# Kernel tuning notes

Hardware: AMD Instinct MI355X
Metric: run time of the kernel (lower is better)

The kernel has to match this reference:

```python
import jax, jax.numpy as jnp
import numpy as np

N = 50000        # num nodes
E = 800000       # num edges (avg degree 16)
IN_DIM = 64
OUT_DIM = 64
PE_DIM = 24
HEADS = 2
HID = OUT_DIM * HEADS  # 128


def setup_inputs() -> dict:
    key = jax.random.key(0)
    ks = jax.random.split(key, 16)
    std = 0.1  # trunc_normal_(std=0.1) init in the torch module
    return {
        "x": jax.random.normal(ks[0], (N, IN_DIM), jnp.float32),
        "pe_index": jax.random.randint(ks[1], (2, E), 0, N, jnp.int32),
        "pe_val": jax.random.normal(ks[2], (E, PE_DIM), jnp.float32),
        # edge-weight MLP (blocks): input proj, one residual FFN block, final proj
        "W_in": jax.random.normal(ks[3], (PE_DIM, HID), jnp.float32) * std,
        "b_in": jnp.zeros((HID,), jnp.float32),
        "W1": jax.random.normal(ks[4], (HID, HID), jnp.float32) * std,
        "b1": jnp.zeros((HID,), jnp.float32),
        "W2": jax.random.normal(ks[5], (HID, HID), jnp.float32) * std,
        "b2": jnp.zeros((HID,), jnp.float32),
        "W_fin": jax.random.normal(ks[6], (HID, HID), jnp.float32) * std,
        "b_fin": jnp.zeros((HID,), jnp.float32),
        # node feature -> multi-head projection
        "W_x": jax.random.normal(ks[7], (IN_DIM, HID), jnp.float32) * std,
        "b_x": jnp.zeros((HID,), jnp.float32),
        # per-head output bias
        "head_bias": jnp.zeros((1, HEADS, OUT_DIM), jnp.float32),
        # final out projection
        "W_out": jax.random.normal(ks[8], (HID, OUT_DIM), jnp.float32) * std,
        "b_out": jnp.zeros((OUT_DIM,), jnp.float32),
    }


def _edge_mlp(pe, W_in, b_in, W1, b1, W2, b2, W_fin, b_fin):
    # Linear(pe_dim->hid), then residual block [GELU, Linear, GELU, Linear, +res], then Linear(hid->hid)
    g = lambda t: jax.nn.gelu(t, approximate=False)  # torch nn.GELU default = exact erf
    x0 = pe @ W_in + b_in                     # [E, HID]
    h = g(x0) @ W1 + b1
    h = g(h) @ W2 + b2
    x0 = h + x0                               # ResidualLayer: x + x_res
    return x0 @ W_fin + b_fin                 # [E, HID]


def reference(x, pe_index, pe_val, W_in, b_in, W1, b1, W2, b2, W_fin, b_fin,
              W_x, b_x, head_bias, W_out, b_out):
    tgt = pe_index[0]  # messages aggregate to edge_index[0]
    src = pe_index[1]
    score = _edge_mlp(pe_val, W_in, b_in, W1, b1, W2, b2, W_fin, b_fin)
    score = score.reshape(-1, HEADS, OUT_DIM)                 # [E, H, D]
    xh = (x @ W_x + b_x).reshape(-1, HEADS, OUT_DIM)          # [N, H, D]
    msg = xh[src] * score                                     # gather-multiply
    wV = jax.ops.segment_sum(msg, tgt, num_segments=N)        # scatter-add [N, H, D]
    deg = jax.ops.segment_sum(jnp.ones((msg.shape[0],), jnp.float32), tgt, num_segments=N)
    wV = wV / jnp.maximum(deg, 1.0)[:, None, None]            # average=True -> mean aggregation
    h = (wV + head_bias).reshape(-1, HEADS * OUT_DIM)
    return h @ W_out + b_out                                  # out_proj: [N, OUT_DIM]
```

## Files before the change

kernel.cpp:

```cpp
#include <hip/hip_runtime.h>
#include <hip/hip_bf16.h>
#include <math.h>

#define NN 50000
#define EE 800000
#define HID 128
#define PED 24
#define IND 64
#define OUTD 64
#define EBLK 64
#define AKS 136

typedef short bf16x8 __attribute__((ext_vector_type(8)));
typedef float f32x4 __attribute__((ext_vector_type(4)));

__device__ __forceinline__ float gelu_fast(float x) {
    float z = fabsf(x) * 0.70710678118654752440f;
    float t = __builtin_amdgcn_rcpf(1.0f + 0.3275911f * z);
    float poly = t * (0.254829592f +
                 t * (-0.284496736f +
                 t * (1.421413741f +
                 t * (-1.453152027f +
                 t * 1.061405429f))));
    float e = __expf(-z * z);
    float erfa = 1.0f - poly * e;
    float s = copysignf(erfa, x);
    return 0.5f * x * (1.0f + s);
}
__device__ __forceinline__ unsigned short f2bf(float f) {
    unsigned int u = __float_as_uint(f);
    u = (u + 0x7fffu + ((u >> 16) & 1u)) >> 16;
    return (unsigned short)u;
}
__device__ __forceinline__ unsigned int pkbf2(float a, float b) {
    __hip_bfloat162 h = __float22bfloat162_rn(make_float2(a, b));
    return *reinterpret_cast<unsigned int*>(&h);
}
__device__ __forceinline__ float bflo(unsigned int u) {
    return __uint_as_float(u << 16);
}
__device__ __forceinline__ float bfhi(unsigned int u) {
    return __uint_as_float(u & 0xffff0000u);
}

__global__ __launch_bounds__(256) void xh_kernel(
    const float* __restrict__ x, const float* __restrict__ W_x,
    const float* __restrict__ b_x, unsigned short* __restrict__ xhb) {
    int gid = blockIdx.x * 256 + threadIdx.x;
    int n = gid >> 5;
    int q = gid & 31;
    if (n >= NN) return;
    const float* xr = x + (size_t)n * IND;
    float4 acc = *(const float4*)&b_x[q * 4];
#pragma unroll 8
    for (int k = 0; k < IND; k++) {
        float xk = xr[k];
        float4 w = *(const float4*)&W_x[k * HID + q * 4];
        acc.x += xk * w.x; acc.y += xk * w.y;
        acc.z += xk * w.z; acc.w += xk * w.w;
    }
    uint2 p;
    p.x = pkbf2(acc.x, acc.y);
    p.y = pkbf2(acc.z, acc.w);
    ((uint2*)&xhb[(size_t)n * HID])[q] = p;
}

__global__ __launch_bounds__(256) void prep_kernel(
    const float* __restrict__ W_in, const float* __restrict__ W1,
    const float* __restrict__ W2, const float* __restrict__ Wf,
    unsigned short* __restrict__ WT_in, unsigned short* __restrict__ WT1,
    unsigned short* __restrict__ WT2, unsigned short* __restrict__ WTf) {
    int idx = blockIdx.x * 256 + threadIdx.x;
    if (idx < 4096) {
        int j = idx >> 5, k = idx & 31;
        WT_in[idx] = f2bf(k < PED ? W_in[k * HID + j] : 0.f);
    } else if (idx < 4096 + 16384) {
        int i = idx - 4096; int j = i >> 7, k = i & 127;
        WT1[i] = f2bf(W1[k * HID + j]);
    } else if (idx < 4096 + 32768) {
        int i = idx - 4096 - 16384; int j = i >> 7, k = i & 127;
        WT2[i] = f2bf(W2[k * HID + j]);
    } else if (idx < 4096 + 49152) {
        int i = idx - 4096 - 32768; int j = i >> 7, k = i & 127;
        WTf[i] = f2bf(Wf[k * HID + j]);
    }
}

__global__ __launch_bounds__(256) void hist_kernel(const int* __restrict__ pe_idx,
                                                   int* __restrict__ cnt) {
    int e = blockIdx.x * 256 + threadIdx.x;
    if (e < EE) atomicAdd(&cnt[pe_idx[e]], 1);
}

__global__ __launch_bounds__(1024) void scan_kernel(const int* __restrict__ cnt,
                                                    int* __restrict__ woff) {
    __shared__ int s_w[16];
    int tid = threadIdx.x;
    const int chunk = (NN + 1023) / 1024;
    int base = tid * chunk;
    int end = base + chunk; if (end > NN) end = NN;
    int s = 0;
    for (int i = base; i < end; i++) s += cnt[i];
    int v = s;
    int lane = tid & 63, wid = tid >> 6;
#pragma unroll
    for (int d = 1; d < 64; d <<= 1) {
        int u = __shfl_up(v, d, 64);
        if (lane >= d) v += u;
    }
    if (lane == 63) s_w[wid] = v;
    __syncthreads();
    if (tid < 16) {
        int wv = s_w[tid];
#pragma unroll
        for (int d = 1; d < 16; d <<= 1) {
            int u = __shfl_up(wv, d, 64);
            if (tid >= d) wv += u;
        }
        s_w[tid] = wv;
    }
    __syncthreads();
    int exc = v - s + (wid ? s_w[wid - 1] : 0);
    int run = exc;
    for (int i = base; i < end; i++) { woff[i] = run; run += cnt[i]; }
}

__global__ __launch_bounds__(256) void scatter_kernel(const int* __restrict__ pe_idx,
                                                      int* __restrict__ woff,
                                                      int* __restrict__ perm) {
    int e = blockIdx.x * 256 + threadIdx.x;
    if (e < EE) {
        int t = pe_idx[e];
        int p = atomicAdd(&woff[t], 1);
        perm[p] = e;
    }
}

__global__ __launch_bounds__(256, 3) void edge_kernel(
    const float* __restrict__ pe_val, const int* __restrict__ pe_idx,
    const int* __restrict__ perm, const unsigned short* __restrict__ xhb,
    const unsigned short* __restrict__ WT_in, const unsigned short* __restrict__ WT1,
    const unsigned short* __restrict__ WT2, const unsigned short* __restrict__ WTf,
    const float* __restrict__ b_in, const float* __restrict__ b1,
    const float* __restrict__ b2, const float* __restrict__ bfin,
    float* __restrict__ wV) {
    __shared__ unsigned short s_act[EBLK][AKS];
    __shared__ __align__(16) unsigned short s_W[HID][AKS];
    __shared__ int s_eid[EBLK], s_tgt[EBLK], s_src[EBLK];
    float* s_msg = (float*)&s_W[0][0];

    const int tid = threadIdx.x;
    const int lane = tid & 63;
    const int w = tid >> 6;
    const int l15 = lane & 15;
    const int quad = lane >> 4;
    const long b0 = (long)blockIdx.x * EBLK;

    if (tid < EBLK) {
        int eid = perm[b0 + tid];
        s_eid[tid] = eid;
        s_tgt[tid] = pe_idx[eid];
        s_src[tid] = pe_idx[EE + eid];
    }
#pragma unroll
    for (int i = 0; i < 8; i++) {
        int idx = tid + i * 256; int r = idx >> 4, seg = idx & 15;
        *(uint4*)&s_W[r][seg * 8] = *(const uint4*)&WT1[r * HID + seg * 8];
    }
    __syncthreads();
#pragma unroll
    for (int i = 0; i < 8; i++) {
        int idx = tid + i * 256; int e = idx >> 5, k = idx & 31;
        float v = (k < PED) ? pe_val[(size_t)s_eid[e] * PED + k] : 0.f;
        s_act[e][k] = f2bf(v);
    }
    __syncthreads();

    f32x4 C[2][4];
    f32x4 x0s[2][4];
    const f32x4 z4 = {0.f, 0.f, 0.f, 0.f};

    {
        bf16x8 a0 = *(const bf16x8*)&WT_in[((2 * w + 0) * 16 + l15) * 32 + quad * 8];
        bf16x8 a1 = *(const bf16x8*)&WT_in[((2 * w + 1) * 16 + l15) * 32 + quad * 8];
#pragma unroll
        for (int u = 0; u < 4; u++) {
            bf16x8 bfr = *(const bf16x8*)&s_act[u * 16 + l15][quad * 8];
            C[0][u] = __builtin_amdgcn_mfma_f32_16x16x32_bf16(a0, bfr, z4, 0, 0, 0);
            C[1][u] = __builtin_amdgcn_mfma_f32_16x16x32_bf16(a1, bfr, z4, 0, 0, 0);
        }
    }
    __syncthreads();
#pragma unroll
    for (int t = 0; t < 2; t++) {
        int ch0 = (2 * w + t) * 16 + quad * 4;
        float4 bb = *(const float4*)&b_in[ch0];
#pragma unroll
        for (int u = 0; u < 4; u++) {
            int e = u * 16 + l15;
            f32x4 c = C[t][u];
            c[0] += bb.x; c[1] += bb.y; c[2] += bb.z; c[3] += bb.w;
            x0s[t][u] = c;
            uint2 p;
            p.x = pkbf2(gelu_fast(c[0]), gelu_fast(c[1]));
            p.y = pkbf2(gelu_fast(c[2]), gelu_fast(c[3]));
            *(uint2*)&s_act[e][ch0] = p;
        }
    }
    __syncthreads();

#define GEMM128()                                                              \
    {                                                                          \
        _Pragma("unroll") for (int t = 0; t < 2; t++)                          \
            _Pragma("unroll") for (int u = 0; u < 4; u++) C[t][u] = z4;        \
        _Pragma("unroll") for (int ks = 0; ks < 4; ks++) {                     \
            bf16x8 a0 = *(const bf16x8*)&s_W[(2 * w + 0) * 16 + l15]           \
                                            [ks * 32 + quad * 8];              \
            bf16x8 a1 = *(const bf16x8*)&s_W[(2 * w + 1) * 16 + l15]           \
                                            [ks * 32 + quad * 8];              \
            _Pragma("unroll") for (int u = 0; u < 4; u++) {                    \
                bf16x8 bfr = *(const bf16x8*)&s_act[u * 16 + l15]              \
                                                   [ks * 32 + quad * 8];       \
                C[0][u] = __builtin_amdgcn_mfma_f32_16x16x32_bf16(a0, bfr,     \
                                                                  C[0][u], 0, 0, 0); \
                C[1][u] = __builtin_amdgcn_mfma_f32_16x16x32_bf16(a1, bfr,     \
                                                                  C[1][u], 0, 0, 0); \
            }                                                                  \
        }                                                                      \
    }

#define STAGE_W(WT)                                                            \
    _Pragma("unroll") for (int i = 0; i < 8; i++) {                            \
        int idx = tid + i * 256; int r = idx >> 4, seg = idx & 15;             \
        *(uint4*)&s_W[r][seg * 8] = *(const uint4*)&(WT)[r * HID + seg * 8];   \
    }

    GEMM128();
    __syncthreads();
#pragma unroll
    for (int t = 0; t < 2; t++) {
        int ch0 = (2 * w + t) * 16 + quad * 4;
        float4 bb = *(const float4*)&b1[ch0];
#pragma unroll
        for (int u = 0; u < 4; u++) {
            int e = u * 16 + l15;
            f32x4 c = C[t][u];
            uint2 p;
            p.x = pkbf2(gelu_fast(c[0] + bb.x), gelu_fast(c[1] + bb.y));
            p.y = pkbf2(gelu_fast(c[2] + bb.z), gelu_fast(c[3] + bb.w));
            *(uint2*)&s_act[e][ch0] = p;
        }
    }
    STAGE_W(WT2);
    __syncthreads();

    GEMM128();
    __syncthreads();
#pragma unroll
    for (int t = 0; t < 2; t++) {
        int ch0 = (2 * w + t) * 16 + quad * 4;
        float4 bb = *(const float4*)&b2[ch0];
#pragma unroll
        for (int u = 0; u < 4; u++) {
            int e = u * 16 + l15;
            f32x4 c = C[t][u];
            f32x4 x0 = x0s[t][u];
            uint2 p;
            p.x = pkbf2(c[0] + bb.x + x0[0], c[1] + bb.y + x0[1]);
            p.y = pkbf2(c[2] + bb.z + x0[2], c[3] + bb.w + x0[3]);
            *(uint2*)&s_act[e][ch0] = p;
        }
    }
    STAGE_W(WTf);
    __syncthreads();

    GEMM128();
    __syncthreads();
#pragma unroll
    for (int t = 0; t < 2; t++) {
        int ch0 = (2 * w + t) * 16 + quad * 4;
        float4 bb = *(const float4*)&bfin[ch0];
#pragma unroll
        for (int u = 0; u < 4; u++) {
            int e = u * 16 + l15;
            f32x4 c = C[t][u];
            uint2 p;
            p.x = pkbf2(c[0] + bb.x, c[1] + bb.y);
            p.y = pkbf2(c[2] + bb.z, c[3] + bb.w);
            *(uint2*)&s_act[e][ch0] = p;
        }
    }
    __syncthreads();

#pragma unroll
    for (int i = 0; i < 8; i++) {
        int idx = tid + i * 256;
        int e = idx >> 5, c4 = idx & 31;
        int src = s_src[e];
        uint2 xv = ((const uint2*)&xhb[(size_t)src * HID])[c4];
        uint2 sv = *(const uint2*)&s_act[e][c4 * 4];
        float4 m;
        m.x = bflo(xv.x) * bflo(sv.x);
        m.y = bfhi(xv.x) * bfhi(sv.x);
        m.z = bflo(xv.y) * bflo(sv.y);
        m.w = bfhi(xv.y) * bfhi(sv.y);
        *(float4*)&s_msg[e * HID + c4 * 4] = m;
    }
    __syncthreads();

    {
        const int h = tid >> 7;
        const int c = tid & 127;
        const int e0h = h * 32;
        float acc = 0.f;
        int prev = s_tgt[e0h];
        bool firstseg = true;
        for (int e = e0h; e < e0h + 32; e++) {
            int t = s_tgt[e];
            if (t != prev) {
                if (firstseg) atomicAdd(&wV[(size_t)prev * HID + c], acc);
                else          wV[(size_t)prev * HID + c] = acc;
                firstseg = false;
                acc = 0.f;
                prev = t;
            }
            acc += s_msg[e * HID + c];
        }
        atomicAdd(&wV[(size_t)prev * HID + c], acc);
    }
#undef GEMM128
#undef STAGE_W
}

__global__ __launch_bounds__(256) void out_kernel(
    const float* __restrict__ wV, const int* __restrict__ cnt,
    const float* __restrict__ head_bias, const float* __restrict__ W_out,
    const float* __restrict__ b_out, float* __restrict__ out) {
    int gid = blockIdx.x * 256 + threadIdx.x;
    int n = gid >> 4;
    int q = gid & 15;
    if (n >= NN) return;
    float inv = 1.0f / fmaxf((float)cnt[n], 1.0f);
    const float* wr = wV + (size_t)n * HID;
    float4 acc = *(const float4*)&b_out[q * 4];
#pragma unroll 4
    for (int k = 0; k < HID; k++) {
        float hv = wr[k] * inv + head_bias[k];
        float4 wv4 = *(const float4*)&W_out[k * OUTD + q * 4];
        acc.x += hv * wv4.x; acc.y += hv * wv4.y;
        acc.z += hv * wv4.z; acc.w += hv * wv4.w;
    }
    *(float4*)&out[(size_t)n * OUTD + q * 4] = acc;
}

extern "C" void kernel_launch(void* const* d_in, const int* in_sizes, int n_in,
                              void* d_out, int out_size, void* d_ws, size_t ws_size,
                              hipStream_t stream) {
    const float* x      = (const float*)d_in[0];
    const int*   pe_idx = (const int*)d_in[1];
    const float* pe_val = (const float*)d_in[2];
    const float* W_in   = (const float*)d_in[3];
    const float* b_in   = (const float*)d_in[4];
    const float* W1     = (const float*)d_in[5];
    const float* b1     = (const float*)d_in[6];
    const float* W2     = (const float*)d_in[7];
    const float* b2     = (const float*)d_in[8];
    const float* Wf     = (const float*)d_in[9];
    const float* bfin   = (const float*)d_in[10];
    const float* W_x    = (const float*)d_in[11];
    const float* b_x    = (const float*)d_in[12];
    const float* hb     = (const float*)d_in[13];
    const float* W_out  = (const float*)d_in[14];
    const float* b_out  = (const float*)d_in[15];
    float* out = (float*)d_out;

    float* wV   = (float*)d_ws;
    int*   cnt  = (int*)(wV + (size_t)NN * HID);
    int*   woff = cnt + NN;
    int*   perm = woff + NN;
    unsigned short* WT_in = (unsigned short*)(perm + EE);
    unsigned short* WT1   = WT_in + 128 * 32;
    unsigned short* WT2   = WT1 + 128 * 128;
    unsigned short* WTf   = WT2 + 128 * 128;
    unsigned short* xhb   = WTf + 128 * 128;

    hipMemsetAsync(wV, 0, ((size_t)NN * HID + NN) * sizeof(float), stream);

    hist_kernel<<<(EE + 255) / 256, 256, 0, stream>>>(pe_idx, cnt);
    scan_kernel<<<1, 1024, 0, stream>>>(cnt, woff);
    scatter_kernel<<<(EE + 255) / 256, 256, 0, stream>>>(pe_idx, woff, perm);
    prep_kernel<<<208, 256, 0, stream>>>(W_in, W1, W2, Wf, WT_in, WT1, WT2, WTf);
    xh_kernel<<<(NN * 32 + 255) / 256, 256, 0, stream>>>(x, W_x, b_x, xhb);

    edge_kernel<<<EE / EBLK, 256, 0, stream>>>(pe_val, pe_idx, perm, xhb,
                                               WT_in, WT1, WT2, WTf,
                                               b_in, b1, b2, bfin, wV);

    out_kernel<<<(NN * 16 + 255) / 256, 256, 0, stream>>>(wV, cnt, hb, W_out,
                                                          b_out, out);
}
```

Baseline: 691.9 us.

## Fuse prep kernels, double edge tile, use tanh GELU, fold biases into MFMA

```diff
diff --git a/kernel.cpp b/kernel.cpp
--- a/kernel.cpp
+++ b/kernel.cpp
@@ -8,24 +8,17 @@
 #define PED 24
 #define IND 64
 #define OUTD 64
-#define EBLK 64
+#define EBLK 128
 #define AKS 136
 
 typedef short bf16x8 __attribute__((ext_vector_type(8)));
 typedef float f32x4 __attribute__((ext_vector_type(4)));
 
 __device__ __forceinline__ float gelu_fast(float x) {
-    float z = fabsf(x) * 0.70710678118654752440f;
-    float t = __builtin_amdgcn_rcpf(1.0f + 0.3275911f * z);
-    float poly = t * (0.254829592f +
-                 t * (-0.284496736f +
-                 t * (1.421413741f +
-                 t * (-1.453152027f +
-                 t * 1.061405429f))));
-    float e = __expf(-z * z);
-    float erfa = 1.0f - poly * e;
-    float s = copysignf(erfa, x);
-    return 0.5f * x * (1.0f + s);
+    float x2 = x * x;
+    float t = __builtin_fmaf(x2, -0.07135481627f, -1.5957691216f);
+    float e = __expf(x * t);
+    return x * __builtin_amdgcn_rcpf(1.0f + e);
 }
 __device__ __forceinline__ unsigned short f2bf(float f) {
     unsigned int u = __float_as_uint(f);
@@ -43,46 +36,49 @@
     return __uint_as_float(u & 0xffff0000u);
 }
 
-__global__ __launch_bounds__(256) void xh_kernel(
+__global__ __launch_bounds__(256) void pre_kernel(
     const float* __restrict__ x, const float* __restrict__ W_x,
-    const float* __restrict__ b_x, unsigned short* __restrict__ xhb) {
-    int gid = blockIdx.x * 256 + threadIdx.x;
-    int n = gid >> 5;
-    int q = gid & 31;
-    if (n >= NN) return;
-    const float* xr = x + (size_t)n * IND;
-    float4 acc = *(const float4*)&b_x[q * 4];
-#pragma unroll 8
-    for (int k = 0; k < IND; k++) {
-        float xk = xr[k];
-        float4 w = *(const float4*)&W_x[k * HID + q * 4];
-        acc.x += xk * w.x; acc.y += xk * w.y;
-        acc.z += xk * w.z; acc.w += xk * w.w;
-    }
-    uint2 p;
-    p.x = pkbf2(acc.x, acc.y);
-    p.y = pkbf2(acc.z, acc.w);
-    ((uint2*)&xhb[(size_t)n * HID])[q] = p;
-}
-
-__global__ __launch_bounds__(256) void prep_kernel(
+    const float* __restrict__ b_x, unsigned short* __restrict__ xhb,
     const float* __restrict__ W_in, const float* __restrict__ W1,
     const float* __restrict__ W2, const float* __restrict__ Wf,
     unsigned short* __restrict__ WT_in, unsigned short* __restrict__ WT1,
-    unsigned short* __restrict__ WT2, unsigned short* __restrict__ WTf) {
-    int idx = blockIdx.x * 256 + threadIdx.x;
-    if (idx < 4096) {
-        int j = idx >> 5, k = idx & 31;
-        WT_in[idx] = f2bf(k < PED ? W_in[k * HID + j] : 0.f);
-    } else if (idx < 4096 + 16384) {
-        int i = idx - 4096; int j = i >> 7, k = i & 127;
-        WT1[i] = f2bf(W1[k * HID + j]);
-    } else if (idx < 4096 + 32768) {
-        int i = idx - 4096 - 16384; int j = i >> 7, k = i & 127;
-        WT2[i] = f2bf(W2[k * HID + j]);
-    } else if (idx < 4096 + 49152) {
-        int i = idx - 4096 - 32768; int j = i >> 7, k = i & 127;
-        WTf[i] = f2bf(Wf[k * HID + j]);
+    unsigned short* __restrict__ WT2, unsigned short* __restrict__ WTf,
+    float* __restrict__ wV, int* __restrict__ cnt) {
+    int bx = blockIdx.x;
+    if (bx < 6250) {
+        int gid = bx * 256 + threadIdx.x;
+        int n = gid >> 5;
+        int q = gid & 31;
+        *(float4*)&wV[(size_t)n * HID + q * 4] = make_float4(0.f, 0.f, 0.f, 0.f);
+        const float* xr = x + (size_t)n * IND;
+        float4 acc = *(const float4*)&b_x[q * 4];
+#pragma unroll 8
+        for (int k = 0; k < IND; k++) {
+            float xk = xr[k];
+            float4 w = *(const float4*)&W_x[k * HID + q * 4];
+            acc.x += xk * w.x; acc.y += xk * w.y;
+            acc.z += xk * w.z; acc.w += xk * w.w;
+        }
+        uint2 p;
+        p.x = pkbf2(acc.x, acc.y);
+        p.y = pkbf2(acc.z, acc.w);
+        ((uint2*)&xhb[(size_t)n * HID])[q] = p;
+    } else {
+        int idx = (bx - 6250) * 256 + threadIdx.x;
+        if (idx < NN) cnt[idx] = 0;
+        if (idx < 4096) {
+            int j = idx >> 5, k = idx & 31;
+            WT_in[idx] = f2bf(k < PED ? W_in[k * HID + j] : 0.f);
+        } else if (idx < 4096 + 16384) {
+            int i = idx - 4096; int j = i >> 7, k = i & 127;
+            WT1[i] = f2bf(W1[k * HID + j]);
+        } else if (idx < 4096 + 32768) {
+            int i = idx - 4096 - 16384; int j = i >> 7, k = i & 127;
+            WT2[i] = f2bf(W2[k * HID + j]);
+        } else if (idx < 4096 + 49152) {
+            int i = idx - 4096 - 32768; int j = i >> 7, k = i & 127;
+            WTf[i] = f2bf(Wf[k * HID + j]);
+        }
     }
 }
 
@@ -136,7 +132,7 @@
     }
 }
 
-__global__ __launch_bounds__(256, 3) void edge_kernel(
+__global__ __launch_bounds__(512, 4) void edge_kernel(
     const float* __restrict__ pe_val, const int* __restrict__ pe_idx,
     const int* __restrict__ perm, const unsigned short* __restrict__ xhb,
     const unsigned short* __restrict__ WT_in, const unsigned short* __restrict__ WT1,
@@ -144,7 +140,7 @@
     const float* __restrict__ b_in, const float* __restrict__ b1,
     const float* __restrict__ b2, const float* __restrict__ bfin,
     float* __restrict__ wV) {
-    __shared__ unsigned short s_act[EBLK][AKS];
+    __shared__ __align__(16) unsigned short s_act[EBLK][AKS];
     __shared__ __align__(16) unsigned short s_W[HID][AKS];
     __shared__ int s_eid[EBLK], s_tgt[EBLK], s_src[EBLK];
     float* s_msg = (float*)&s_W[0][0];
@@ -152,6 +148,9 @@
     const int tid = threadIdx.x;
     const int lane = tid & 63;
     const int w = tid >> 6;
+    const int cg = w & 3;
+    const int eh = w >> 2;
+    const int ebase = eh * 64;
     const int l15 = lane & 15;
     const int quad = lane >> 4;
     const long b0 = (long)blockIdx.x * EBLK;
@@ -163,43 +162,45 @@
         s_src[tid] = pe_idx[EE + eid];
     }
 #pragma unroll
-    for (int i = 0; i < 8; i++) {
-        int idx = tid + i * 256; int r = idx >> 4, seg = idx & 15;
+    for (int i = 0; i < 4; i++) {
+        int idx = tid + i * 512; int r = idx >> 4, seg = idx & 15;
         *(uint4*)&s_W[r][seg * 8] = *(const uint4*)&WT1[r * HID + seg * 8];
     }
     __syncthreads();
 #pragma unroll
-    for (int i = 0; i < 8; i++) {
-        int idx = tid + i * 256; int e = idx >> 5, k = idx & 31;
-        float v = (k < PED) ? pe_val[(size_t)s_eid[e] * PED + k] : 0.f;
-        s_act[e][k] = f2bf(v);
+    for (int i = 0; i < 4; i++) {
+        int idx = tid + i * 512; int e = idx >> 4, k2 = idx & 15;
+        float2 v = make_float2(0.f, 0.f);
+        if (k2 < 12) v = *(const float2*)&pe_val[(size_t)s_eid[e] * PED + k2 * 2];
+        *(unsigned int*)&s_act[e][k2 * 2] = pkbf2(v.x, v.y);
     }
     __syncthreads();
 
     f32x4 C[2][4];
     f32x4 x0s[2][4];
-    const f32x4 z4 = {0.f, 0.f, 0.f, 0.f};
 
     {
-        bf16x8 a0 = *(const bf16x8*)&WT_in[((2 * w + 0) * 16 + l15) * 32 + quad * 8];
-        bf16x8 a1 = *(const bf16x8*)&WT_in[((2 * w + 1) * 16 + l15) * 32 + quad * 8];
+        float4 ba = *(const float4*)&b_in[(2 * cg + 0) * 16 + quad * 4];
+        float4 bb = *(const float4*)&b_in[(2 * cg + 1) * 16 + quad * 4];
+        f32x4 ci0 = {ba.x, ba.y, ba.z, ba.w};
+        f32x4 ci1 = {bb.x, bb.y, bb.z, bb.w};
+        bf16x8 a0 = *(const bf16x8*)&WT_in[((2 * cg + 0) * 16 + l15) * 32 + quad * 8];
+        bf16x8 a1 = *(const bf16x8*)&WT_in[((2 * cg + 1) * 16 + l15) * 32 + quad * 8];
 #pragma unroll
         for (int u = 0; u < 4; u++) {
-            bf16x8 bfr = *(const bf16x8*)&s_act[u * 16 + l15][quad * 8];
-            C[0][u] = __builtin_amdgcn_mfma_f32_16x16x32_bf16(a0, bfr, z4, 0, 0, 0);
-            C[1][u] = __builtin_amdgcn_mfma_f32_16x16x32_bf16(a1, bfr, z4, 0, 0, 0);
+            bf16x8 bfr = *(const bf16x8*)&s_act[ebase + u * 16 + l15][quad * 8];
+            C[0][u] = __builtin_amdgcn_mfma_f32_16x16x32_bf16(a0, bfr, ci0, 0, 0, 0);
+            C[1][u] = __builtin_amdgcn_mfma_f32_16x16x32_bf16(a1, bfr, ci1, 0, 0, 0);
         }
     }
     __syncthreads();
 #pragma unroll
     for (int t = 0; t < 2; t++) {
-        int ch0 = (2 * w + t) * 16 + quad * 4;
-        float4 bb = *(const float4*)&b_in[ch0];
+        int ch0 = (2 * cg + t) * 16 + quad * 4;
 #pragma unroll
         for (int u = 0; u < 4; u++) {
-            int e = u * 16 + l15;
+            int e = ebase + u * 16 + l15;
             f32x4 c = C[t][u];
-            c[0] += bb.x; c[1] += bb.y; c[2] += bb.z; c[3] += bb.w;
             x0s[t][u] = c;
             uint2 p;
             p.x = pkbf2(gelu_fast(c[0]), gelu_fast(c[1]));
@@ -209,17 +210,22 @@
     }
     __syncthreads();
 
-#define GEMM128()                                                              \
+#define GEMM128(BIAS)                                                          \
     {                                                                          \
-        _Pragma("unroll") for (int t = 0; t < 2; t++)                          \
-            _Pragma("unroll") for (int u = 0; u < 4; u++) C[t][u] = z4;        \
+        float4 ba_ = *(const float4*)&(BIAS)[(2 * cg + 0) * 16 + quad * 4];    \
+        float4 bb_ = *(const float4*)&(BIAS)[(2 * cg + 1) * 16 + quad * 4];    \
+        f32x4 ci0 = {ba_.x, ba_.y, ba_.z, ba_.w};                              \
+        f32x4 ci1 = {bb_.x, bb_.y, bb_.z, bb_.w};                              \
+        _Pragma("unroll") for (int u = 0; u < 4; u++) {                        \
+            C[0][u] = ci0; C[1][u] = ci1;                                      \
+        }                                                                      \
         _Pragma("unroll") for (int ks = 0; ks < 4; ks++) {                     \
-            bf16x8 a0 = *(const bf16x8*)&s_W[(2 * w + 0) * 16 + l15]           \
+            bf16x8 a0 = *(const bf16x8*)&s_W[(2 * cg + 0) * 16 + l15]          \
                                             [ks * 32 + quad * 8];              \
-            bf16x8 a1 = *(const bf16x8*)&s_W[(2 * w + 1) * 16 + l15]           \
+            bf16x8 a1 = *(const bf16x8*)&s_W[(2 * cg + 1) * 16 + l15]          \
                                             [ks * 32 + quad * 8];              \
             _Pragma("unroll") for (int u = 0; u < 4; u++) {                    \
-                bf16x8 bfr = *(const bf16x8*)&s_act[u * 16 + l15]              \
+                bf16x8 bfr = *(const bf16x8*)&s_act[ebase + u * 16 + l15]      \
                                                    [ks * 32 + quad * 8];       \
                 C[0][u] = __builtin_amdgcn_mfma_f32_16x16x32_bf16(a0, bfr,     \
                                                                   C[0][u], 0, 0, 0); \
@@ -230,74 +236,76 @@
     }
 
 #define STAGE_W(WT)                                                            \
-    _Pragma("unroll") for (int i = 0; i < 8; i++) {                            \
-        int idx = tid + i * 256; int r = idx >> 4, seg = idx & 15;             \
+    _Pragma("unroll") for (int i = 0; i < 4; i++) {                            \
+        int idx = tid + i * 512; int r = idx >> 4, seg = idx & 15;             \
         *(uint4*)&s_W[r][seg * 8] = *(const uint4*)&(WT)[r * HID + seg * 8];   \
     }
 
-    GEMM128();
+    GEMM128(b1);
     __syncthreads();
 #pragma unroll
     for (int t = 0; t < 2; t++) {
-        int ch0 = (2 * w + t) * 16 + quad * 4;
-        float4 bb = *(const float4*)&b1[ch0];
+        int ch0 = (2 * cg + t) * 16 + quad * 4;
 #pragma unroll
         for (int u = 0; u < 4; u++) {
-            int e = u * 16 + l15;
+            int e = ebase + u * 16 + l15;
             f32x4 c = C[t][u];
             uint2 p;
-            p.x = pkbf2(gelu_fast(c[0] + bb.x), gelu_fast(c[1] + bb.y));
-            p.y = pkbf2(gelu_fast(c[2] + bb.z), gelu_fast(c[3] + bb.w));
+            p.x = pkbf2(gelu_fast(c[0]), gelu_fast(c[1]));
+            p.y = pkbf2(gelu_fast(c[2]), gelu_fast(c[3]));
             *(uint2*)&s_act[e][ch0] = p;
         }
     }
     STAGE_W(WT2);
     __syncthreads();
 
-    GEMM128();
+    GEMM128(b2);
     __syncthreads();
 #pragma unroll
     for (int t = 0; t < 2; t++) {
-        int ch0 = (2 * w + t) * 16 + quad * 4;
-        float4 bb = *(const float4*)&b2[ch0];
+        int ch0 = (2 * cg + t) * 16 + quad * 4;
 #pragma unroll
         for (int u = 0; u < 4; u++) {
-            int e = u * 16 + l15;
+            int e = ebase + u * 16 + l15;
             f32x4 c = C[t][u];
             f32x4 x0 = x0s[t][u];
             uint2 p;
-            p.x = pkbf2(c[0] + bb.x + x0[0], c[1] + bb.y + x0[1]);
-            p.y = pkbf2(c[2] + bb.z + x0[2], c[3] + bb.w + x0[3]);
+            p.x = pkbf2(c[0] + x0[0], c[1] + x0[1]);
+            p.y = pkbf2(c[2] + x0[2], c[3] + x0[3]);
             *(uint2*)&s_act[e][ch0] = p;
         }
     }
     STAGE_W(WTf);
     __syncthreads();
 
-    GEMM128();
+    GEMM128(bfin);
+    uint2 xva[4];
+#pragma unroll
+    for (int i = 0; i < 4; i++) {
+        int idx = tid + i * 512; int e = idx >> 5, c4 = idx & 31;
+        xva[i] = ((const uint2*)&xhb[(size_t)s_src[e] * HID])[c4];
+    }
     __syncthreads();
 #pragma unroll
     for (int t = 0; t < 2; t++) {
-        int ch0 = (2 * w + t) * 16 + quad * 4;
-        float4 bb = *(const float4*)&bfin[ch0];
+        int ch0 = (2 * cg + t) * 16 + quad * 4;
 #pragma unroll
         for (int u = 0; u < 4; u++) {
-            int e = u * 16 + l15;
+            int e = ebase + u * 16 + l15;
             f32x4 c = C[t][u];
             uint2 p;
-            p.x = pkbf2(c[0] + bb.x, c[1] + bb.y);
-            p.y = pkbf2(c[2] + bb.z, c[3] + bb.w);
+            p.x = pkbf2(c[0], c[1]);
+            p.y = pkbf2(c[2], c[3]);
             *(uint2*)&s_act[e][ch0] = p;
         }
     }
     __syncthreads();
 
 #pragma unroll
-    for (int i = 0; i < 8; i++) {
-        int idx = tid + i * 256;
+    for (int i = 0; i < 4; i++) {
+        int idx = tid + i * 512;
         int e = idx >> 5, c4 = idx & 31;
-        int src = s_src[e];
-        uint2 xv = ((const uint2*)&xhb[(size_t)src * HID])[c4];
+        uint2 xv = xva[i];
         uint2 sv = *(const uint2*)&s_act[e][c4 * 4];
         float4 m;
         m.x = bflo(xv.x) * bflo(sv.x);
@@ -306,25 +314,68 @@
         m.w = bfhi(xv.y) * bfhi(sv.y);
         *(float4*)&s_msg[e * HID + c4 * 4] = m;
     }
-    __syncthreads();
-
-    {
+    uint2 xvb[4];
+#pragma unroll
+    for (int i = 0; i < 4; i++) {
+        int idx = tid + (4 + i) * 512; int e = idx >> 5, c4 = idx & 31;
+        xvb[i] = ((const uint2*)&xhb[(size_t)s_src[e] * HID])[c4];
+    }
+    __syncthreads();
+
+    if (tid < 256) {
         const int h = tid >> 7;
         const int c = tid & 127;
-        const int e0h = h * 32;
+        const int e0 = h * 32;
         float acc = 0.f;
-        int prev = s_tgt[e0h];
+        int prev = s_tgt[e0];
         bool firstseg = true;
-        for (int e = e0h; e < e0h + 32; e++) {
-            int t = s_tgt[e];
-            if (t != prev) {
+        for (int e = e0; e < e0 + 32; e++) {
+            int tg = s_tgt[e];
+            if (tg != prev) {
                 if (firstseg) atomicAdd(&wV[(size_t)prev * HID + c], acc);
                 else          wV[(size_t)prev * HID + c] = acc;
                 firstseg = false;
                 acc = 0.f;
-                prev = t;
+                prev = tg;
             }
             acc += s_msg[e * HID + c];
+        }
+        atomicAdd(&wV[(size_t)prev * HID + c], acc);
+    }
+    __syncthreads();
+
+#pragma unroll
+    for (int i = 0; i < 4; i++) {
+        int idx = tid + (4 + i) * 512;
+        int e = idx >> 5, c4 = idx & 31;
+        uint2 xv = xvb[i];
+        uint2 sv = *(const uint2*)&s_act[e][c4 * 4];
+        float4 m;
+        m.x = bflo(xv.x) * bflo(sv.x);
+        m.y = bfhi(xv.x) * bfhi(sv.x);
+        m.z = bflo(xv.y) * bflo(sv.y);
+        m.w = bfhi(xv.y) * bfhi(sv.y);
+        *(float4*)&s_msg[(e - 64) * HID + c4 * 4] = m;
+    }
+    __syncthreads();
+
+    if (tid < 256) {
+        const int h = tid >> 7;
+        const int c = tid & 127;
+        const int e0 = 64 + h * 32;
+        float acc = 0.f;
+        int prev = s_tgt[e0];
+        bool firstseg = true;
+        for (int e = e0; e < e0 + 32; e++) {
+            int tg = s_tgt[e];
+            if (tg != prev) {
+                if (firstseg) atomicAdd(&wV[(size_t)prev * HID + c], acc);
+                else          wV[(size_t)prev * HID + c] = acc;
+                firstseg = false;
+                acc = 0.f;
+                prev = tg;
+            }
+            acc += s_msg[(e - 64) * HID + c];
         }
         atomicAdd(&wV[(size_t)prev * HID + c], acc);
     }
@@ -384,15 +435,14 @@
     unsigned short* WTf   = WT2 + 128 * 128;
     unsigned short* xhb   = WTf + 128 * 128;
 
-    hipMemsetAsync(wV, 0, ((size_t)NN * HID + NN) * sizeof(float), stream);
-
+    pre_kernel<<<6250 + 208, 256, 0, stream>>>(x, W_x, b_x, xhb,
+                                               W_in, W1, W2, Wf,
+                                               WT_in, WT1, WT2, WTf, wV, cnt);
     hist_kernel<<<(EE + 255) / 256, 256, 0, stream>>>(pe_idx, cnt);
     scan_kernel<<<1, 1024, 0, stream>>>(cnt, woff);
     scatter_kernel<<<(EE + 255) / 256, 256, 0, stream>>>(pe_idx, woff, perm);
-    prep_kernel<<<208, 256, 0, stream>>>(W_in, W1, W2, Wf, WT_in, WT1, WT2, WTf);
-    xh_kernel<<<(NN * 32 + 255) / 256, 256, 0, stream>>>(x, W_x, b_x, xhb);
-
-    edge_kernel<<<EE / EBLK, 256, 0, stream>>>(pe_val, pe_idx, perm, xhb,
+
+    edge_kernel<<<EE / EBLK, 512, 0, stream>>>(pe_val, pe_idx, perm, xhb,
                                                WT_in, WT1, WT2, WTf,
                                                b_in, b1, b2, bfin, wV);
 
```

New measurement: 632.5 us. -8.6%, faster.
